# Performance work log

Measured on AMD Instinct MI355X. Metric: run time of the kernel, lower is better.

Reference implementation:

```python
import math
import jax, jax.numpy as jnp
import numpy as np

T, D = 1024, 7168
N = 128
A_Q, A_KV = 1536, 512
QK_NOPE, QK_ROPE, V_DIM = 128, 64, 128
QK_HEAD = QK_NOPE + QK_ROPE  # 192
PAD_H = 256                  # padded to multiple of 128 in attn_op
EPS = 1e-6
ROPE_THETA, FACTOR, ORIG_MAX = 10000.0, 40.0, 4096
BETA_FAST, BETA_SLOW = 32, 1


def _yarn_inv_freq():
    """DeepseekScalingRotaryEmbedding (yarn) inverse frequencies, static."""
    dim = QK_ROPE
    pos_freqs = ROPE_THETA ** (np.arange(0, dim, 2, dtype=np.float64) / dim)
    inv_extra = 1.0 / pos_freqs
    inv_inter = 1.0 / (FACTOR * pos_freqs)

    def corr_dim(n_rot):
        return dim * math.log(ORIG_MAX / (n_rot * 2 * math.pi)) / (2 * math.log(ROPE_THETA))

    low = max(math.floor(corr_dim(BETA_FAST)), 0)
    high = min(math.ceil(corr_dim(BETA_SLOW)), dim - 1)
    ramp = np.clip((np.arange(dim // 2, dtype=np.float64) - low) / max(high - low, 1e-3), 0.0, 1.0)
    mask = 1.0 - ramp  # 1 -> extrapolation, 0 -> interpolation
    inv = inv_inter * (1.0 - mask) + inv_extra * mask
    return jnp.asarray(inv, dtype=jnp.float32)

_INV_FREQ = _yarn_inv_freq()
# mscale ratio: yarn_get_mscale(FACTOR, mscale)/yarn_get_mscale(FACTOR, mscale_all_dim) == 1.0
_MSCALE = 1.0


def _apply_rope(positions, x):
    # x: [T, N, QK_ROPE], split (rotate-half) ordering
    ang = positions[:, None].astype(jnp.float32) * _INV_FREQ[None, :]  # [T, 32]
    cos = (jnp.cos(ang) * _MSCALE)[:, None, :]
    sin = (jnp.sin(ang) * _MSCALE)[:, None, :]
    x1, x2 = x[..., : QK_ROPE // 2], x[..., QK_ROPE // 2:]
    return jnp.concatenate([x1 * cos - x2 * sin, x2 * cos + x1 * sin], axis=-1)


def _rms_norm(x, scale):
    var = jnp.mean(x * x, axis=-1, keepdims=True)
    return x * jax.lax.rsqrt(var + EPS) * scale


def setup_inputs() -> dict:
    key = jax.random.key(0)
    ks = jax.random.split(key, 6)
    s = 0.02
    return {
        "x": jax.random.normal(ks[0], (T, D), jnp.float32),
        "positions": jnp.arange(T, dtype=jnp.int32),
        "w_q_down": jax.random.normal(ks[1], (D, A_Q), jnp.float32) * s,
        "q_norm_scale": jnp.ones((A_Q,), jnp.float32),
        "w_q_up": jax.random.normal(ks[2], (A_Q, N, QK_HEAD), jnp.float32) * s,
        "w_kv_down": jax.random.normal(ks[3], (D, A_KV + QK_ROPE), jnp.float32) * s,
        "kv_norm_scale": jnp.ones((A_KV,), jnp.float32),
        "w_kv_up": jax.random.normal(ks[4], (A_KV, N, QK_NOPE + V_DIM), jnp.float32) * s,
        "w_o": jax.random.normal(ks[5], (N, V_DIM, D), jnp.float32) * s,
    }


def reference(x, positions, w_q_down, q_norm_scale, w_q_up, w_kv_down,
              kv_norm_scale, w_kv_up, w_o):
    # ---- q path: down-proj -> RMSNorm -> up-proj -> split RoPE ----
    q_TA = jnp.einsum('td,da->ta', x, w_q_down)
    q_TA = _rms_norm(q_TA, q_norm_scale)
    q_TNH = jnp.einsum('ta,anh->tnh', q_TA, w_q_up)
    q_rope = _apply_rope(positions, q_TNH[..., QK_NOPE:])
    q_TNH = jnp.concatenate([q_TNH[..., :QK_NOPE], q_rope], axis=-1)
    q_TNH = q_TNH * (QK_HEAD ** -0.5)

    # ---- kv path: down-proj -> (rope slice | RMSNorm latent -> up-proj) ----
    kv_SA = jnp.einsum('sd,da->sa', x, w_kv_down)
    k_rope = _apply_rope(positions, kv_SA[..., A_KV:][:, None, :])  # [S,1,64]
    k_rope = jnp.broadcast_to(k_rope, (T, N, QK_ROPE))
    c_SA = _rms_norm(kv_SA[..., :A_KV], kv_norm_scale)
    kv_nope = jnp.einsum('sa,anh->snh', c_SA, w_kv_up)
    k_SNH = jnp.concatenate([kv_nope[..., :QK_NOPE], k_rope], axis=-1)
    v_SNH = kv_nope[..., QK_NOPE:]

    # ---- attention (prefill, causal); zero-pad of head dim does not change dots,
    # but sm_scale uses the PADDED dim (256) as in the original attn_op ----
    sm_scale = PAD_H ** -0.5
    logits = jnp.einsum('tnh,snh->nts', q_TNH, k_SNH) * sm_scale
    t_idx = jnp.arange(T)
    causal = t_idx[:, None] >= t_idx[None, :]  # [T, S]
    logits = jnp.where(causal[None, :, :], logits, jnp.float32(-1e30))
    probs = jax.nn.softmax(logits, axis=-1)
    out_TNH = jnp.einsum('nts,snh->tnh', probs, v_SNH)

    # ---- output projection ----
    o_TD = jnp.einsum('tnh,nhd->td', out_TNH, w_o)
    return o_TD
```

## Files before the change

### kernel.cpp

```cpp
#include <hip/hip_runtime.h>
#include <hip/hip_bf16.h>
#include <math.h>

typedef __attribute__((ext_vector_type(4))) float f32x4;
typedef __attribute__((ext_vector_type(8))) short bf16x8;
typedef __attribute__((ext_vector_type(4))) short bf16x4;

static __device__ __forceinline__ float bf2f(short u){
  unsigned int i = ((unsigned int)(unsigned short)u) << 16;
  return __builtin_bit_cast(float, i);
}
static __device__ __forceinline__ short f2bf(float f){
  unsigned int u = __builtin_bit_cast(unsigned int, f);
  u += 0x7FFFu + ((u >> 16) & 1u);
  return (short)(u >> 16);
}

#define GLD16(g, l) __builtin_amdgcn_global_load_lds(                         \
    (const __attribute__((address_space(1))) void*)(g),                       \
    (__attribute__((address_space(3))) void*)(l), 16, 0, 0)

template<typename CT, int SPLITS>
__global__ __launch_bounds__(512, 2) void gemm256(const short* __restrict__ A,
                                                  const short* __restrict__ BT,
                                                  CT* __restrict__ C,
                                                  float* __restrict__ P,
                                                  int M, int N, int K)
{
  extern __shared__ __align__(16) char smem[];
  const int tid = threadIdx.x;
  const int w = tid >> 6, lane = tid & 63;
  const int wm = w >> 2, wn = w & 3;
  const int g = lane >> 4, l16 = lane & 15;

  const int per_z = gridDim.x * gridDim.y;
  const int F = (blockIdx.z * gridDim.y + blockIdx.y) * gridDim.x + blockIdx.x;
  const int nwgF = per_z * gridDim.z;
  const int cpxF = nwgF >> 3;
  const int T = (F & 7) * cpxF + (F >> 3);
  const int zz = T / per_z, tt = T % per_z;
  const int m0 = (tt & 3) * 256;
  const int n0 = (tt >> 2) * 256;

  const int Ks   = K / SPLITS;
  const int kbeg = zz * Ks;
  const int NT   = Ks >> 5;

  const int gg = (lane & 3) ^ ((lane >> 2) & 3) ^ ((lane >> 4) & 1);
  const short* aSrc[2]; const short* bSrc[2];
  int ldsOff[2];
  #pragma unroll
  for (int j = 0; j < 2; j++){
    int r = (w + j*8)*16 + (lane >> 2);
    aSrc[j] = A  + (size_t)(m0 + r) * K + kbeg + gg*8;
    bSrc[j] = BT + (size_t)(n0 + r) * K + kbeg + gg*8;
    ldsOff[j] = (w + j*8) * 1024;
  }

  const int sw = ((g ^ (l16 & 3) ^ ((l16 >> 2) & 1)) << 4);

  f32x4 acc[8][4];
  #pragma unroll
  for (int i = 0; i < 8; i++)
    #pragma unroll
    for (int j = 0; j < 4; j++) acc[i][j] = (f32x4){0.f,0.f,0.f,0.f};

  auto stage = [&](int b, int t){
    const int koff = t * 32;
    char* dst = smem + b * 32768;
    #pragma unroll
    for (int j = 0; j < 2; j++){
      GLD16(aSrc[j] + koff, dst + ldsOff[j]);
      GLD16(bSrc[j] + koff, dst + 16384 + ldsOff[j]);
    }
  };

  auto wait_pub = [&](int ahead){
    if (ahead >= 3)      asm volatile("s_waitcnt vmcnt(8)" ::: "memory");
    else if (ahead == 2) asm volatile("s_waitcnt vmcnt(4)" ::: "memory");
    else                 asm volatile("s_waitcnt vmcnt(0)" ::: "memory");
    __builtin_amdgcn_s_barrier();
    asm volatile("" ::: "memory");
  };

  stage(0, 0);
  if (NT > 1) stage(1, 1);
  if (NT > 2) stage(2, 2);
  wait_pub(NT - 1 >= 2 ? (NT > 2 ? 3 : 2) : 1);

  const int arow = wm*128 + l16;
  const int brow = wn*64  + l16;

  for (int t = 0; t < NT; t++){
    const int sl = t & 3;
    if (t + 3 < NT) stage((t + 3) & 3, t + 3);

    const char* base = smem + sl * 32768;
    bf16x8 a[8], bb[4];
    #pragma unroll
    for (int mi = 0; mi < 8; mi++)
      a[mi] = *reinterpret_cast<const bf16x8*>(base + (arow + mi*16)*64 + sw);
    #pragma unroll
    for (int ni = 0; ni < 4; ni++)
      bb[ni] = *reinterpret_cast<const bf16x8*>(base + 16384 + (brow + ni*16)*64 + sw);

    __builtin_amdgcn_s_setprio(1);
    #pragma unroll
    for (int mi = 0; mi < 8; mi++)
      #pragma unroll
      for (int ni = 0; ni < 4; ni++)
        acc[mi][ni] = __builtin_amdgcn_mfma_f32_16x16x32_bf16(a[mi], bb[ni], acc[mi][ni], 0, 0, 0);
    __builtin_amdgcn_s_setprio(0);

    wait_pub(NT - 1 - t);
  }

  #pragma unroll
  for (int mi = 0; mi < 8; mi++){
    int row = m0 + wm*128 + mi*16 + g*4;
    #pragma unroll
    for (int ni = 0; ni < 4; ni++){
      int col = n0 + wn*64 + ni*16 + l16;
      #pragma unroll
      for (int r = 0; r < 4; r++){
        if constexpr (SPLITS > 1){
          P[(size_t)zz*M*N + (size_t)(row+r)*N + col] = acc[mi][ni][r];
        } else if constexpr (sizeof(CT) == 4){
          C[(size_t)(row+r)*N + col] = acc[mi][ni][r];
        } else {
          C[(size_t)(row+r)*N + col] = f2bf(acc[mi][ni][r]);
        }
      }
    }
  }
}

template<typename CT, int SPLITS>
__global__ __launch_bounds__(256) void gemm_bt(const short* __restrict__ A,
                                               const short* __restrict__ BT,
                                               CT* __restrict__ C,
                                               float* __restrict__ P,
                                               int M, int N, int K)
{
  __shared__ __align__(16) short As[2][128*32];
  __shared__ __align__(16) short Bs[2][128*32];
  const int tid = threadIdx.x;
  const int f   = blockIdx.y * 8 + blockIdx.x;
  const int nwg = 8 * gridDim.y;
  const int cpx = nwg >> 3;
  const int t   = (f & 7) * cpx + (f >> 3);
  const int m0  = (t & 7) * 128;
  const int n0  = (t >> 3) * 128;
  const int w = tid >> 6, lane = tid & 63;
  const int wr = w >> 1, wc = w & 1;
  const int g = lane >> 4, l16 = lane & 15;

  const int Ks   = K / SPLITS;
  const int kbeg = blockIdx.z * Ks;
  const int kend = kbeg + Ks;

  const int sr = lane >> 2;
  const int kc = (lane & 3) << 3;
  const int arow0 = m0 + w*16 + sr;
  const int arow1 = m0 + (w+4)*16 + sr;
  int brow0 = n0 + w*16 + sr;      if (brow0 >= N) brow0 = N - 1;
  int brow1 = n0 + (w+4)*16 + sr;  if (brow1 >= N) brow1 = N - 1;
  const short* aG0 = A  + (size_t)arow0 * K + kc;
  const short* aG1 = A  + (size_t)arow1 * K + kc;
  const short* bG0 = BT + (size_t)brow0 * K + kc;
  const short* bG1 = BT + (size_t)brow1 * K + kc;
  char* aL = (char*)As;
  char* bL = (char*)Bs;

  auto stage = [&](int buf, int k0){
    char* ab = aL + buf*8192;
    char* bb = bL + buf*8192;
    GLD16(aG0 + k0, ab + (w  )*1024);
    GLD16(aG1 + k0, ab + (w+4)*1024);
    GLD16(bG0 + k0, bb + (w  )*1024);
    GLD16(bG1 + k0, bb + (w+4)*1024);
  };

  f32x4 acc[4][4];
  #pragma unroll
  for (int i=0;i<4;i++)
    #pragma unroll
    for (int j=0;j<4;j++) acc[i][j] = (f32x4){0.f,0.f,0.f,0.f};

  stage(0, kbeg);
  __syncthreads();

  int cur = 0;
  for (int k0 = kbeg; k0 < kend; k0 += 32){
    if (k0 + 32 < kend) stage(cur ^ 1, k0 + 32);

    const char* ar = aL + cur*8192;
    const char* br = bL + cur*8192;
    bf16x8 af[4], bfm[4];
    #pragma unroll
    for (int mi=0;mi<4;mi++){
      int row = wr*64 + mi*16 + l16;
      af[mi] = *reinterpret_cast<const bf16x8*>(ar + row*64 + g*16);
    }
    #pragma unroll
    for (int ni=0;ni<4;ni++){
      int row = wc*64 + ni*16 + l16;
      bfm[ni] = *reinterpret_cast<const bf16x8*>(br + row*64 + g*16);
    }
    #pragma unroll
    for (int mi=0;mi<4;mi++)
      #pragma unroll
      for (int ni=0;ni<4;ni++)
        acc[mi][ni] = __builtin_amdgcn_mfma_f32_16x16x32_bf16(af[mi], bfm[ni], acc[mi][ni], 0, 0, 0);

    __syncthreads();
    cur ^= 1;
  }

  #pragma unroll
  for (int mi=0;mi<4;mi++){
    int row = m0 + wr*64 + mi*16 + g*4;
    #pragma unroll
    for (int ni=0;ni<4;ni++){
      int col = n0 + wc*64 + ni*16 + l16;
      if (col < N){
        #pragma unroll
        for (int r=0;r<4;r++){
          if constexpr (SPLITS > 1){
            P[(size_t)blockIdx.z*M*N + (size_t)(row+r)*N + col] = acc[mi][ni][r];
          } else if constexpr (sizeof(CT) == 4){
            C[(size_t)(row+r)*N + col] = acc[mi][ni][r];
          } else {
            C[(size_t)(row+r)*N + col] = f2bf(acc[mi][ni][r]);
          }
        }
      }
    }
  }
}

template<int NP>
__global__ __launch_bounds__(256) void reduceN(const float* __restrict__ p,
                                               float* __restrict__ out,
                                               int n4, int mn4)
{
  int i = blockIdx.x * 256 + threadIdx.x;
  const int stride = gridDim.x * 256;
  for (; i < n4; i += stride){
    f32x4 s = reinterpret_cast<const f32x4*>(p)[i];
    #pragma unroll
    for (int z = 1; z < NP; z++)
      s = s + reinterpret_cast<const f32x4*>(p)[(size_t)z*mn4 + i];
    reinterpret_cast<f32x4*>(out)[i] = s;
  }
}

__global__ __launch_bounds__(256) void transpose_f32_bf16(const float* __restrict__ src,
                                                          short* __restrict__ dst,
                                                          int R, int C)
{
  __shared__ float tl[64][68];
  const int tid = threadIdx.x;
  const int r0 = blockIdx.y * 64, c0 = blockIdx.x * 64;
  {
    const int lr = tid >> 4, lc = (tid & 15) << 2;
    #pragma unroll
    for (int p = 0; p < 4; p++){
      int row = p*16 + lr;
      f32x4 v = *reinterpret_cast<const f32x4*>(src + (size_t)(r0+row)*C + c0 + lc);
      *reinterpret_cast<f32x4*>(&tl[row][lc]) = v;
    }
  }
  __syncthreads();
  {
    const int n = tid >> 2, ks = (tid & 3) << 4;
    short tmp[16];
    #pragma unroll
    for (int j = 0; j < 16; j++) tmp[j] = f2bf(tl[ks + j][n]);
    short* d = dst + (size_t)(c0+n)*R + r0 + ks;
    *reinterpret_cast<bf16x8*>(d)     = *reinterpret_cast<bf16x8*>(&tmp[0]);
    *reinterpret_cast<bf16x8*>(d + 8) = *reinterpret_cast<bf16x8*>(&tmp[8]);
  }
}

__global__ __launch_bounds__(256) void conv_f32_bf16(const float* __restrict__ src,
                                                     short* __restrict__ dst, int n4)
{
  int i = blockIdx.x * 256 + threadIdx.x;
  const int stride = gridDim.x * 256;
  for (; i < n4; i += stride){
    f32x4 v = reinterpret_cast<const f32x4*>(src)[i];
    bf16x4 h; h[0]=f2bf(v[0]); h[1]=f2bf(v[1]); h[2]=f2bf(v[2]); h[3]=f2bf(v[3]);
    reinterpret_cast<bf16x4*>(dst)[i] = h;
  }
}

__global__ __launch_bounds__(256) void mla_rmsnorm_bf(const float* __restrict__ dc,
                                                      const float* __restrict__ scale,
                                                      short* __restrict__ out)
{
  const int t = blockIdx.x;
  const float* row = dc + (size_t)t * 2112;
  float ss = 0.f;
  for (int i = threadIdx.x; i < 1536; i += 256){ float v = row[i]; ss += v*v; }
  #pragma unroll
  for (int off = 32; off >= 1; off >>= 1) ss += __shfl_xor(ss, off);
  __shared__ float red[4];
  if ((threadIdx.x & 63) == 0) red[threadIdx.x >> 6] = ss;
  __syncthreads();
  ss = red[0] + red[1] + red[2] + red[3];
  const float rs = 1.0f / sqrtf(ss / 1536.f + 1e-6f);
  for (int i = threadIdx.x; i < 1536; i += 256)
    out[(size_t)t*1536 + i] = f2bf(row[i] * rs * scale[i]);
}

__device__ __forceinline__ void yarn_cs(int pos, int j, float& c, float& s){
  const double dim = 64.0;
  double pf = pow(10000.0, (2.0*(double)j)/dim);
  double inv_extra = 1.0/pf;
  double inv_inter = inv_extra/40.0;
  double lo = floor(dim*log(4096.0/(32.0*2.0*M_PI))/(2.0*log(10000.0)));
  double hi = ceil (dim*log(4096.0/(       2.0*M_PI))/(2.0*log(10000.0)));
  if (lo < 0.0) lo = 0.0;
  if (hi > dim - 1.0) hi = dim - 1.0;
  double denom = hi - lo; if (denom < 0.001) denom = 0.001;
  double ramp = ((double)j - lo)/denom;
  ramp = ramp < 0.0 ? 0.0 : (ramp > 1.0 ? 1.0 : ramp);
  double mask = 1.0 - ramp;
  float invf = (float)(inv_inter*(1.0 - mask) + inv_extra*mask);
  float ang = (float)pos * invf;
  c = cosf(ang); s = sinf(ang);
}

__global__ __launch_bounds__(256) void mla_rope_q(short* __restrict__ qb,
                                                  const int* __restrict__ positions)
{
  const int t = blockIdx.x;
  __shared__ float cs[32], sn[32];
  if (threadIdx.x < 32){
    float c, s; yarn_cs(positions[t], threadIdx.x, c, s);
    cs[threadIdx.x] = c; sn[threadIdx.x] = s;
  }
  __syncthreads();
  const float f = 0.004510548978043951f;
  short* row = qb + (size_t)t * 24576;
  for (int idx = threadIdx.x; idx < 128*160; idx += 256){
    int n = idx / 160, e = idx % 160;
    short* p = row + n*192;
    if (e < 128){
      p[e] = f2bf(bf2f(p[e]) * f);
    } else {
      int j = e - 128;
      float x1 = bf2f(p[128+j]), x2 = bf2f(p[160+j]);
      p[128+j] = f2bf((x1*cs[j] - x2*sn[j]) * f);
      p[160+j] = f2bf((x2*cs[j] + x1*sn[j]) * f);
    }
  }
}

__global__ __launch_bounds__(256) void mla_kv_post(const float* __restrict__ dc,
                                                   const float* __restrict__ scale,
                                                   const int* __restrict__ positions,
                                                   short* __restrict__ cbuf,
                                                   short* __restrict__ krope)
{
  const int t = blockIdx.x;
  const float* row = dc + (size_t)t * 2112 + 1536;
  float ss = 0.f;
  for (int i = threadIdx.x; i < 512; i += 256){ float v = row[i]; ss += v*v; }
  #pragma unroll
  for (int off = 32; off >= 1; off >>= 1) ss += __shfl_xor(ss, off);
  __shared__ float red[4];
  if ((threadIdx.x & 63) == 0) red[threadIdx.x >> 6] = ss;
  __syncthreads();
  ss = red[0] + red[1] + red[2] + red[3];
  const float rs = 1.0f / sqrtf(ss / 512.f + 1e-6f);
  for (int i = threadIdx.x; i < 512; i += 256)
    cbuf[(size_t)t*512 + i] = f2bf(row[i] * rs * scale[i]);
  if (threadIdx.x < 32){
    int j = threadIdx.x;
    float c, s; yarn_cs(positions[t], j, c, s);
    float x1 = row[512 + j], x2 = row[544 + j];
    krope[(size_t)t*64 + j]      = f2bf(x1*c - x2*s);
    krope[(size_t)t*64 + 32 + j] = f2bf(x2*c + x1*s);
  }
}

__global__ __launch_bounds__(512) void mla_attn2(const short* __restrict__ qb,
                                                 const short* __restrict__ kvup,
                                                 const short* __restrict__ krope,
                                                 short* __restrict__ attn_out)
{
  const int f = blockIdx.x;
  const int xcd = f & 7, pos = f >> 3;
  const int n  = xcd*16 + (pos >> 2);
  const int pair = pos & 3;
  const int tid = threadIdx.x, w = tid >> 6, lane = tid & 63;
  const int g = lane >> 4, l16 = lane & 15;

  __shared__ __align__(16) short Klds[64*192];
  __shared__ __align__(16) short Vlds[128*64];
  __shared__ __align__(16) short Plds[8][16*64];
  char* KB = (char*)Klds; char* VB = (char*)Vlds; char* PB = (char*)Plds[w];

  bf16x8 kpre[3], vpre[2];

  int kS[3], kHB[3];
  #pragma unroll
  for (int c=0;c<3;c++){
    int lin = c*512 + tid;
    kS[c] = lin / 24; kHB[c] = (lin % 24) * 8;
  }
  int vS[2], vVB[2], vROT[2];
  #pragma unroll
  for (int c=0;c<2;c++){
    int lin = c*512 + tid;
    vS[c] = lin >> 4; vVB[c] = (lin & 15) << 3; vROT[c] = (lin & 15) & 7;
  }

  auto stage_load = [&](int S0){
    #pragma unroll
    for (int c=0;c<3;c++){
      const short* src = (kHB[c] < 128)
        ? kvup  + (size_t)(S0 + kS[c])*32768 + n*256 + kHB[c]
        : krope + (size_t)(S0 + kS[c])*64 + (kHB[c]-128);
      kpre[c] = *reinterpret_cast<const bf16x8*>(src);
    }
    #pragma unroll
    for (int c=0;c<2;c++)
      vpre[c] = *reinterpret_cast<const bf16x8*>(kvup + (size_t)(S0 + vS[c])*32768 + n*256 + 128 + vVB[c]);
  };
  auto stage_write = [&](){
    #pragma unroll
    for (int c=0;c<3;c++){
      unsigned byte = (unsigned)(kS[c]*384 + kHB[c]*2) ^ ((unsigned)(kS[c]&7)<<4);
      *reinterpret_cast<bf16x8*>(KB + byte) = kpre[c];
    }
    #pragma unroll
    for (int c=0;c<2;c++){
      #pragma unroll
      for (int i=0;i<8;i++){
        int v = vVB[c] + i;
        unsigned byte = (unsigned)(v*128 + ((vS[c]*2 + vROT[c]*16) & 127));
        *reinterpret_cast<short*>(VB + byte) = vpre[c][i];
      }
    }
  };

  stage_load(0);
  stage_write();
  __syncthreads();

  #pragma unroll
  for (int p = 0; p < 2; p++){
    const int qtl = p ? (7 - pair) : pair;
    const int t0 = qtl * 128;
    const int last = 2*qtl + 1;

    bf16x8 qf[6];
    {
      const size_t qrow = (size_t)(t0 + w*16 + l16) * 24576 + (size_t)n * 192;
      #pragma unroll
      for (int c=0;c<6;c++)
        qf[c] = *reinterpret_cast<const bf16x8*>(qb + qrow + c*32 + g*8);
    }
    f32x4 o[8];
    #pragma unroll
    for (int i=0;i<8;i++) o[i] = (f32x4){0.f,0.f,0.f,0.f};
    float m[4], l[4];
    #pragma unroll
    for (int r=0;r<4;r++){ m[r] = -1e30f; l[r] = 0.f; }

    for (int sb = 0; sb <= last; sb++){
      const bool more = (sb < last) || (p == 0);
      if (more) stage_load((sb < last) ? (sb+1)*64 : 0);

      f32x4 S[4];
      __builtin_amdgcn_s_setprio(1);
      #pragma unroll
      for (int st=0; st<4; st++){
        f32x4 sacc = (f32x4){0.f,0.f,0.f,0.f};
        int srow = st*16 + l16;
        #pragma unroll
        for (int c=0;c<6;c++){
          unsigned byte = (unsigned)(srow*384 + c*64 + g*16) ^ ((unsigned)(srow&7)<<4);
          bf16x8 kf = *reinterpret_cast<const bf16x8*>(KB + byte);
          sacc = __builtin_amdgcn_mfma_f32_16x16x32_bf16(qf[c], kf, sacc, 0, 0, 0);
        }
        S[st] = sacc;
      }
      __builtin_amdgcn_s_setprio(0);

      if (sb >= 2*qtl){
        #pragma unroll
        for (int st=0;st<4;st++){
          int sg = sb*64 + st*16 + l16;
          #pragma unroll
          for (int r=0;r<4;r++){
            int qg = t0 + w*16 + g*4 + r;
            if (sg > qg) S[st][r] = -1e30f;
          }
        }
      }
      float alpha[4];
      #pragma unroll
      for (int r=0;r<4;r++){
        float mx = fmaxf(fmaxf(S[0][r],S[1][r]), fmaxf(S[2][r],S[3][r]));
        #pragma unroll
        for (int off=8; off>=1; off>>=1) mx = fmaxf(mx, __shfl_xor(mx, off));
        float mnew = fmaxf(m[r], mx);
        alpha[r] = __expf(m[r] - mnew);
        m[r] = mnew;
        l[r] *= alpha[r];
      }
      #pragma unroll
      for (int st=0;st<4;st++)
        #pragma unroll
        for (int r=0;r<4;r++)
          S[st][r] = __expf(S[st][r] - m[r]);
      #pragma unroll
      for (int r=0;r<4;r++){
        float sum = S[0][r]+S[1][r]+S[2][r]+S[3][r];
        #pragma unroll
        for (int off=8; off>=1; off>>=1) sum += __shfl_xor(sum, off);
        l[r] += sum;
      }
      #pragma unroll
      for (int vt=0; vt<8; vt++)
        #pragma unroll
        for (int r=0;r<4;r++) o[vt][r] *= alpha[r];

      #pragma unroll
      for (int st=0;st<4;st++){
        #pragma unroll
        for (int r=0;r<4;r++){
          int qrow = g*4 + r, scol = st*16 + l16;
          unsigned byte = (unsigned)(qrow*128 + scol*2) ^ ((unsigned)(qrow&7)<<4);
          *reinterpret_cast<short*>(PB + byte) = f2bf(S[st][r]);
        }
      }
      bf16x8 pf[2];
      #pragma unroll
      for (int c=0;c<2;c++){
        unsigned byte = (unsigned)(l16*128 + (c*32 + g*8)*2) ^ ((unsigned)(l16&7)<<4);
        pf[c] = *reinterpret_cast<const bf16x8*>(PB + byte);
      }
      __builtin_amdgcn_s_setprio(1);
      #pragma unroll
      for (int vt=0; vt<8; vt++){
        #pragma unroll
        for (int c=0;c<2;c++){
          int vrow = vt*16 + l16;
          int rot = (vrow >> 3) & 7;
          unsigned byte = (unsigned)(vrow*128 + ((c*64 + g*16 + rot*16) & 127));
          bf16x8 vf = *reinterpret_cast<const bf16x8*>(VB + byte);
          o[vt] = __builtin_amdgcn_mfma_f32_16x16x32_bf16(pf[c], vf, o[vt], 0, 0, 0);
        }
      }
      __builtin_amdgcn_s_setprio(0);

      if (more){
        __syncthreads();
        stage_write();
        __syncthreads();
      }
    }

    #pragma unroll
    for (int r=0;r<4;r++){
      float inv = 1.f / l[r];
      int t = t0 + w*16 + g*4 + r;
      #pragma unroll
      for (int vt=0;vt<8;vt++){
        int v = vt*16 + l16;
        attn_out[(size_t)t*16384 + n*128 + v] = f2bf(o[vt][r] * inv);
      }
    }
  }
}

extern "C" void kernel_launch(void* const* d_in, const int* in_sizes, int n_in,
                              void* d_out, int out_size, void* d_ws, size_t ws_size,
                              hipStream_t stream) {
  const float* x            = (const float*)d_in[0];
  const int*   positions    = (const int*)  d_in[1];
  const float* w_q_down     = (const float*)d_in[2];
  const float* q_norm_scale = (const float*)d_in[3];
  const float* w_q_up       = (const float*)d_in[4];
  const float* w_kv_down    = (const float*)d_in[5];
  const float* kv_norm_scale= (const float*)d_in[6];
  const float* w_kv_up      = (const float*)d_in[7];
  const float* w_o          = (const float*)d_in[8];

  char* p = (char*)d_ws;
  short* xbf   = (short*)p; p += (size_t)1024*7168*2;
  short* wdT   = (short*)p; p += (size_t)2112*7168*2;
  short* wquT  = (short*)p; p += (size_t)24576*1536*2;
  short* wkuT  = (short*)p; p += (size_t)32768*512*2;
  short* woT   = (short*)p; p += (size_t)7168*16384*2;
  float* downC = (float*)p; p += (size_t)1024*2112*4;
  short* qAbf  = (short*)p; p += (size_t)1024*1536*2;
  short* q_b   = (short*)p; p += (size_t)1024*24576*2;
  short* cbuf  = (short*)p; p += (size_t)1024*512*2;
  short* krope = (short*)p; p += (size_t)1024*64*2;
  short* kvup  = (short*)p; p += (size_t)1024*32768*2;
  short* attn_o= (short*)p; p += (size_t)1024*16384*2;

  float* pDown = (float*)q_b;
  float* pWo   = (float*)d_ws;

  hipFuncSetAttribute(reinterpret_cast<const void*>(&gemm256<short,1>),
                      hipFuncAttributeMaxDynamicSharedMemorySize, 131072);
  hipFuncSetAttribute(reinterpret_cast<const void*>(&gemm256<float,2>),
                      hipFuncAttributeMaxDynamicSharedMemorySize, 131072);

  dim3 blk(256);
  conv_f32_bf16<<<2048, blk, 0, stream>>>(x, xbf, 1024*7168/4);
  transpose_f32_bf16<<<dim3(24, 112),  blk, 0, stream>>>(w_q_down,  wdT,                     7168, 1536);
  transpose_f32_bf16<<<dim3(9, 112),   blk, 0, stream>>>(w_kv_down, wdT + (size_t)1536*7168, 7168, 576);
  transpose_f32_bf16<<<dim3(384, 24),  blk, 0, stream>>>(w_q_up,    wquT,                    1536, 24576);
  transpose_f32_bf16<<<dim3(512, 8),   blk, 0, stream>>>(w_kv_up,   wkuT,                    512,  32768);
  transpose_f32_bf16<<<dim3(112, 256), blk, 0, stream>>>(w_o,       woT,                     16384, 7168);

  gemm_bt<float, 4><<<dim3(8, 17, 4), blk, 0, stream>>>(xbf, wdT, (float*)nullptr, pDown, 1024, 2112, 7168);
  reduceN<4><<<1024, blk, 0, stream>>>(pDown, downC, 1024*2112/4, 1024*2112/4);
  mla_rmsnorm_bf<<<1024, blk, 0, stream>>>(downC, q_norm_scale, qAbf);
  mla_kv_post<<<1024, blk, 0, stream>>>(downC, kv_norm_scale, positions, cbuf, krope);

  gemm256<short, 1><<<dim3(4, 96), dim3(512), 131072, stream>>>(qAbf, wquT, q_b, nullptr, 1024, 24576, 1536);
  mla_rope_q<<<1024, blk, 0, stream>>>(q_b, positions);
  gemm256<short, 1><<<dim3(4, 128), dim3(512), 131072, stream>>>(cbuf, wkuT, kvup, nullptr, 1024, 32768, 512);

  mla_attn2<<<512, dim3(512), 0, stream>>>(q_b, kvup, krope, attn_o);

  gemm256<float, 2><<<dim3(4, 28, 2), dim3(512), 131072, stream>>>(attn_o, woT, (float*)nullptr, pWo, 1024, 7168, 16384);
  reduceN<2><<<2048, blk, 0, stream>>>(pWo, (float*)d_out, 1024*7168/4, 1024*7168/4);
}
```

Measured before the change: 883.1 us.

## Split GEMM k-step into two phases interleaving prefetch with MFMA

Restructures the GEMM main loop into two half-phases. Each phase loads half of the A fragments, issues half of the next global-to-LDS prefetch, and runs half of the MFMAs, separated by extra barriers. This is a ping-pong style schedule meant to interleave memory issue with compute and cut fragment register pressure. It adds three extra barriers per k-step, which may cost more than the overlap gains.

```diff
diff --git a/kernel.cpp b/kernel.cpp
--- a/kernel.cpp
+++ b/kernel.cpp
@@ -65,54 +65,71 @@
     #pragma unroll
     for (int j = 0; j < 4; j++) acc[i][j] = (f32x4){0.f,0.f,0.f,0.f};
 
-  auto stage = [&](int b, int t){
+  auto stage_half = [&](int b, int t, int j){
     const int koff = t * 32;
     char* dst = smem + b * 32768;
-    #pragma unroll
-    for (int j = 0; j < 2; j++){
-      GLD16(aSrc[j] + koff, dst + ldsOff[j]);
-      GLD16(bSrc[j] + koff, dst + 16384 + ldsOff[j]);
-    }
+    GLD16(aSrc[j] + koff, dst + ldsOff[j]);
+    GLD16(bSrc[j] + koff, dst + 16384 + ldsOff[j]);
   };
 
-  auto wait_pub = [&](int ahead){
-    if (ahead >= 3)      asm volatile("s_waitcnt vmcnt(8)" ::: "memory");
-    else if (ahead == 2) asm volatile("s_waitcnt vmcnt(4)" ::: "memory");
-    else                 asm volatile("s_waitcnt vmcnt(0)" ::: "memory");
+  stage_half(0, 0, 0); stage_half(0, 0, 1);
+  if (NT > 1){ stage_half(1, 1, 0); stage_half(1, 1, 1); }
+  if (NT > 2){ stage_half(2, 2, 0); stage_half(2, 2, 1); }
+  {
+    if (NT > 2)      asm volatile("s_waitcnt vmcnt(8)" ::: "memory");
+    else if (NT > 1) asm volatile("s_waitcnt vmcnt(4)" ::: "memory");
+    else             asm volatile("s_waitcnt vmcnt(0)" ::: "memory");
     __builtin_amdgcn_s_barrier();
     asm volatile("" ::: "memory");
-  };
-
-  stage(0, 0);
-  if (NT > 1) stage(1, 1);
-  if (NT > 2) stage(2, 2);
-  wait_pub(NT - 1 >= 2 ? (NT > 2 ? 3 : 2) : 1);
+  }
 
   const int arow = wm*128 + l16;
   const int brow = wn*64  + l16;
 
   for (int t = 0; t < NT; t++){
     const int sl = t & 3;
-    if (t + 3 < NT) stage((t + 3) & 3, t + 3);
-
+    const bool pf = (t + 3 < NT);
     const char* base = smem + sl * 32768;
-    bf16x8 a[8], bb[4];
-    #pragma unroll
-    for (int mi = 0; mi < 8; mi++)
+    bf16x8 a[4], bb[4];
+
+    #pragma unroll
+    for (int mi = 0; mi < 4; mi++)
       a[mi] = *reinterpret_cast<const bf16x8*>(base + (arow + mi*16)*64 + sw);
     #pragma unroll
     for (int ni = 0; ni < 4; ni++)
       bb[ni] = *reinterpret_cast<const bf16x8*>(base + 16384 + (brow + ni*16)*64 + sw);
-
+    if (pf) stage_half((t + 3) & 3, t + 3, 0);
+    __builtin_amdgcn_s_barrier();
     __builtin_amdgcn_s_setprio(1);
     #pragma unroll
-    for (int mi = 0; mi < 8; mi++)
+    for (int mi = 0; mi < 4; mi++)
       #pragma unroll
       for (int ni = 0; ni < 4; ni++)
         acc[mi][ni] = __builtin_amdgcn_mfma_f32_16x16x32_bf16(a[mi], bb[ni], acc[mi][ni], 0, 0, 0);
     __builtin_amdgcn_s_setprio(0);
-
-    wait_pub(NT - 1 - t);
+    __builtin_amdgcn_s_barrier();
+
+    #pragma unroll
+    for (int mi = 0; mi < 4; mi++)
+      a[mi] = *reinterpret_cast<const bf16x8*>(base + (arow + (mi+4)*16)*64 + sw);
+    if (pf) stage_half((t + 3) & 3, t + 3, 1);
+    __builtin_amdgcn_s_barrier();
+    __builtin_amdgcn_s_setprio(1);
+    #pragma unroll
+    for (int mi = 0; mi < 4; mi++)
+      #pragma unroll
+      for (int ni = 0; ni < 4; ni++)
+        acc[mi+4][ni] = __builtin_amdgcn_mfma_f32_16x16x32_bf16(a[mi], bb[ni], acc[mi+4][ni], 0, 0, 0);
+    __builtin_amdgcn_s_setprio(0);
+
+    {
+      const int ahead = NT - 1 - t;
+      if (ahead >= 3)      asm volatile("s_waitcnt vmcnt(8)" ::: "memory");
+      else if (ahead == 2) asm volatile("s_waitcnt vmcnt(4)" ::: "memory");
+      else                 asm volatile("s_waitcnt vmcnt(0)" ::: "memory");
+    }
+    __builtin_amdgcn_s_barrier();
+    asm volatile("" ::: "memory");
   }
 
   #pragma unroll
```

After: 902.0 us. +2.1%, slower.

## Shrink GEMM tile to 128x256 with triple-buffered LDS for higher occupancy

Applied to the files above, without the earlier changes.

The 256x256 bf16 GEMM kernel becomes a 128x256 tile variant. Each warp now holds a 4x4 MFMA accumulator block instead of 8x4, the LDS ring drops from four 32KB stages to three 24KB stages, and launch bounds allow 4 blocks per CU. This doubles the grid for the q-up, kv-up and output projections, aiming for better CU fill and latency hiding. The cost is lower arithmetic intensity per tile, so more global and LDS traffic per FLOP, and a shallower prefetch depth.

```diff
diff --git a/kernel.cpp b/kernel.cpp
--- a/kernel.cpp
+++ b/kernel.cpp
@@ -21,7 +21,7 @@
     (__attribute__((address_space(3))) void*)(l), 16, 0, 0)
 
 template<typename CT, int SPLITS>
-__global__ __launch_bounds__(512, 2) void gemm256(const short* __restrict__ A,
+__global__ __launch_bounds__(512, 4) void gemm_hn(const short* __restrict__ A,
                                                   const short* __restrict__ BT,
                                                   CT* __restrict__ C,
                                                   float* __restrict__ P,
@@ -39,85 +39,83 @@
   const int cpxF = nwgF >> 3;
   const int T = (F & 7) * cpxF + (F >> 3);
   const int zz = T / per_z, tt = T % per_z;
-  const int m0 = (tt & 3) * 256;
-  const int n0 = (tt >> 2) * 256;
+  const int m0 = (tt & 7) * 128;
+  const int n0 = (tt >> 3) * 256;
 
   const int Ks   = K / SPLITS;
   const int kbeg = zz * Ks;
   const int NT   = Ks >> 5;
 
-  const int gg = (lane & 3) ^ ((lane >> 2) & 3) ^ ((lane >> 4) & 1);
-  const short* aSrc[2]; const short* bSrc[2];
-  int ldsOff[2];
-  #pragma unroll
-  for (int j = 0; j < 2; j++){
-    int r = (w + j*8)*16 + (lane >> 2);
-    aSrc[j] = A  + (size_t)(m0 + r) * K + kbeg + gg*8;
-    bSrc[j] = BT + (size_t)(n0 + r) * K + kbeg + gg*8;
-    ldsOff[j] = (w + j*8) * 1024;
-  }
+  const int rowA = tid >> 2, col4 = tid & 3;
+  const int fA  = (rowA & 3) ^ ((rowA >> 2) & 1);
+  const int ggA = col4 ^ fA;
+  const short* aS  = A  + (size_t)(m0 + rowA)       * K + kbeg + ggA*8;
+  const short* bS0 = BT + (size_t)(n0 + rowA)       * K + kbeg + ggA*8;
+  const short* bS1 = BT + (size_t)(n0 + rowA + 128) * K + kbeg + ggA*8;
+  const int ldsA  = w * 1024;
+  const int ldsB0 = 8192  + w * 1024;
+  const int ldsB1 = 16384 + w * 1024;
 
   const int sw = ((g ^ (l16 & 3) ^ ((l16 >> 2) & 1)) << 4);
 
-  f32x4 acc[8][4];
-  #pragma unroll
-  for (int i = 0; i < 8; i++)
+  f32x4 acc[4][4];
+  #pragma unroll
+  for (int i = 0; i < 4; i++)
     #pragma unroll
     for (int j = 0; j < 4; j++) acc[i][j] = (f32x4){0.f,0.f,0.f,0.f};
 
   auto stage = [&](int b, int t){
     const int koff = t * 32;
-    char* dst = smem + b * 32768;
-    #pragma unroll
-    for (int j = 0; j < 2; j++){
-      GLD16(aSrc[j] + koff, dst + ldsOff[j]);
-      GLD16(bSrc[j] + koff, dst + 16384 + ldsOff[j]);
-    }
-  };
-
-  auto wait_pub = [&](int ahead){
-    if (ahead >= 3)      asm volatile("s_waitcnt vmcnt(8)" ::: "memory");
-    else if (ahead == 2) asm volatile("s_waitcnt vmcnt(4)" ::: "memory");
-    else                 asm volatile("s_waitcnt vmcnt(0)" ::: "memory");
-    __builtin_amdgcn_s_barrier();
-    asm volatile("" ::: "memory");
+    char* dst = smem + b * 24576;
+    GLD16(aS  + koff, dst + ldsA);
+    GLD16(bS0 + koff, dst + ldsB0);
+    GLD16(bS1 + koff, dst + ldsB1);
   };
 
   stage(0, 0);
   if (NT > 1) stage(1, 1);
-  if (NT > 2) stage(2, 2);
-  wait_pub(NT - 1 >= 2 ? (NT > 2 ? 3 : 2) : 1);
-
-  const int arow = wm*128 + l16;
-  const int brow = wn*64  + l16;
-
+  if (NT > 1) asm volatile("s_waitcnt vmcnt(3)" ::: "memory");
+  else        asm volatile("s_waitcnt vmcnt(0)" ::: "memory");
+  __builtin_amdgcn_s_barrier();
+  asm volatile("" ::: "memory");
+
+  const int arow = wm*64 + l16;
+  const int brow = wn*64 + l16;
+
+  int sl = 0, sp = 2;
   for (int t = 0; t < NT; t++){
-    const int sl = t & 3;
-    if (t + 3 < NT) stage((t + 3) & 3, t + 3);
-
-    const char* base = smem + sl * 32768;
-    bf16x8 a[8], bb[4];
-    #pragma unroll
-    for (int mi = 0; mi < 8; mi++)
+    const bool pf = (t + 2 < NT);
+    if (pf) stage(sp, t + 2);
+
+    const char* base = smem + sl * 24576;
+    bf16x8 a[4], bb[4];
+    #pragma unroll
+    for (int mi = 0; mi < 4; mi++)
       a[mi] = *reinterpret_cast<const bf16x8*>(base + (arow + mi*16)*64 + sw);
     #pragma unroll
     for (int ni = 0; ni < 4; ni++)
-      bb[ni] = *reinterpret_cast<const bf16x8*>(base + 16384 + (brow + ni*16)*64 + sw);
+      bb[ni] = *reinterpret_cast<const bf16x8*>(base + 8192 + (brow + ni*16)*64 + sw);
 
     __builtin_amdgcn_s_setprio(1);
     #pragma unroll
-    for (int mi = 0; mi < 8; mi++)
+    for (int mi = 0; mi < 4; mi++)
       #pragma unroll
       for (int ni = 0; ni < 4; ni++)
         acc[mi][ni] = __builtin_amdgcn_mfma_f32_16x16x32_bf16(a[mi], bb[ni], acc[mi][ni], 0, 0, 0);
     __builtin_amdgcn_s_setprio(0);
 
-    wait_pub(NT - 1 - t);
-  }
-
-  #pragma unroll
-  for (int mi = 0; mi < 8; mi++){
-    int row = m0 + wm*128 + mi*16 + g*4;
+    if (pf) asm volatile("s_waitcnt vmcnt(3)" ::: "memory");
+    else    asm volatile("s_waitcnt vmcnt(0)" ::: "memory");
+    __builtin_amdgcn_s_barrier();
+    asm volatile("" ::: "memory");
+
+    sl = (sl == 2) ? 0 : sl + 1;
+    sp = (sp == 2) ? 0 : sp + 1;
+  }
+
+  #pragma unroll
+  for (int mi = 0; mi < 4; mi++){
+    int row = m0 + wm*64 + mi*16 + g*4;
     #pragma unroll
     for (int ni = 0; ni < 4; ni++){
       int col = n0 + wn*64 + ni*16 + l16;
@@ -609,10 +607,10 @@
   float* pDown = (float*)q_b;
   float* pWo   = (float*)d_ws;
 
-  hipFuncSetAttribute(reinterpret_cast<const void*>(&gemm256<short,1>),
-                      hipFuncAttributeMaxDynamicSharedMemorySize, 131072);
-  hipFuncSetAttribute(reinterpret_cast<const void*>(&gemm256<float,2>),
-                      hipFuncAttributeMaxDynamicSharedMemorySize, 131072);
+  hipFuncSetAttribute(reinterpret_cast<const void*>(&gemm_hn<short,1>),
+                      hipFuncAttributeMaxDynamicSharedMemorySize, 73728);
+  hipFuncSetAttribute(reinterpret_cast<const void*>(&gemm_hn<float,2>),
+                      hipFuncAttributeMaxDynamicSharedMemorySize, 73728);
 
   dim3 blk(256);
   conv_f32_bf16<<<2048, blk, 0, stream>>>(x, xbf, 1024*7168/4);
@@ -627,12 +625,12 @@
   mla_rmsnorm_bf<<<1024, blk, 0, stream>>>(downC, q_norm_scale, qAbf);
   mla_kv_post<<<1024, blk, 0, stream>>>(downC, kv_norm_scale, positions, cbuf, krope);
 
-  gemm256<short, 1><<<dim3(4, 96), dim3(512), 131072, stream>>>(qAbf, wquT, q_b, nullptr, 1024, 24576, 1536);
+  gemm_hn<short, 1><<<dim3(8, 96), dim3(512), 73728, stream>>>(qAbf, wquT, q_b, nullptr, 1024, 24576, 1536);
   mla_rope_q<<<1024, blk, 0, stream>>>(q_b, positions);
-  gemm256<short, 1><<<dim3(4, 128), dim3(512), 131072, stream>>>(cbuf, wkuT, kvup, nullptr, 1024, 32768, 512);
+  gemm_hn<short, 1><<<dim3(8, 128), dim3(512), 73728, stream>>>(cbuf, wkuT, kvup, nullptr, 1024, 32768, 512);
 
   mla_attn2<<<512, dim3(512), 0, stream>>>(q_b, kvup, krope, attn_o);
 
-  gemm256<float, 2><<<dim3(4, 28, 2), dim3(512), 131072, stream>>>(attn_o, woT, (float*)nullptr, pWo, 1024, 7168, 16384);
+  gemm_hn<float, 2><<<dim3(8, 28, 2), dim3(512), 73728, stream>>>(attn_o, woT, (float*)nullptr, pWo, 1024, 7168, 16384);
   reduceN<2><<<2048, blk, 0, stream>>>(pWo, (float*)d_out, 1024*7168/4, 1024*7168/4);
 }
```

Result: no change. 899.2 us (+1.8%).
